# Kernel tuning notes

Hardware: AMD Instinct MI355X
Metric: run time of the kernel (lower is better)

## Reference

```python
import jax, jax.numpy as jnp
import numpy as np

IMG = 1024.0
POOL = 7
STRIDES = (4, 8, 16, 32)  # levels P2..P5
STDS = jnp.array([0.1, 0.1, 0.2, 0.2], dtype=jnp.float32)  # RCNN_TARGET_STDS


def delta2bbox(rois, deltas):
    # rois: [N,4] (y1,x1,y2,x2) pixels; deltas: [N,4]
    d = deltas * STDS  # means are zero
    y1, x1, y2, x2 = rois[:, 0], rois[:, 1], rois[:, 2], rois[:, 3]
    h = y2 - y1
    w = x2 - x1
    cy = y1 + 0.5 * h + d[:, 0] * h
    cx = x1 + 0.5 * w + d[:, 1] * w
    h = h * jnp.exp(d[:, 2])
    w = w * jnp.exp(d[:, 3])
    b = jnp.stack([cy - 0.5 * h, cx - 0.5 * w, cy + 0.5 * h, cx + 0.5 * w], axis=1)
    return jnp.clip(b, 0.0, IMG)


def crop_level(feat, rois, stride):
    # feat: [H,W,C]; bilinear 7x7 crop (crop_and_resize style)
    H, W, _ = feat.shape
    s = rois / stride
    grid = (jnp.arange(POOL, dtype=jnp.float32) + 0.5) / POOL
    ys = s[:, 0:1] + grid[None, :] * (s[:, 2:3] - s[:, 0:1])  # [N,7]
    xs = s[:, 1:2] + grid[None, :] * (s[:, 3:4] - s[:, 1:2])  # [N,7]
    y0f = jnp.clip(jnp.floor(ys), 0.0, H - 1)
    x0f = jnp.clip(jnp.floor(xs), 0.0, W - 1)
    y0 = y0f.astype(jnp.int32)
    x0 = x0f.astype(jnp.int32)
    y1 = jnp.minimum(y0 + 1, H - 1)
    x1 = jnp.minimum(x0 + 1, W - 1)
    wy = jnp.clip(ys - y0f, 0.0, 1.0)[:, :, None, None]  # [N,7,1,1]
    wx = jnp.clip(xs - x0f, 0.0, 1.0)[:, None, :, None]  # [N,1,7,1]
    g = lambda yi, xi: feat[yi[:, :, None], xi[:, None, :]]  # [N,7,7,C]
    return (g(y0, x0) * (1 - wy) * (1 - wx) + g(y0, x1) * (1 - wy) * wx
            + g(y1, x0) * wy * (1 - wx) + g(y1, x1) * wy * wx)


def pyramid_roi_align(feats, rois):
    h = rois[:, 2] - rois[:, 0]
    w = rois[:, 3] - rois[:, 1]
    lvl = jnp.floor(4.0 + jnp.log2(jnp.sqrt(jnp.maximum(h * w, 1e-6)) / 224.0))
    lvl = jnp.clip(lvl, 2.0, 5.0).astype(jnp.int32)
    pooled = 0.0
    for i, (feat, stride) in enumerate(zip(feats, STRIDES)):
        mask = (lvl == i + 2).astype(feat.dtype)[:, None, None, None]
        pooled = pooled + crop_level(feat, rois, stride) * mask
    return pooled  # [N,7,7,C]


def bbox_head(pooled, i, fc1_w, fc1_b, fc2_w, fc2_b, cls_w, cls_b, reg_w, reg_b):
    n = pooled.shape[0]
    x = pooled.reshape(n, -1)
    h1 = jax.nn.relu(x @ fc1_w[i] + fc1_b[i])
    h2 = jax.nn.relu(h1 @ fc2_w[i] + fc2_b[i])
    logits = h2 @ cls_w[i] + cls_b[i]
    probs = jax.nn.softmax(logits, axis=-1)
    deltas = h2 @ reg_w[i] + reg_b[i]
    return logits, probs, deltas


def setup_inputs() -> dict:
    key = jax.random.key(0)
    ks = jax.random.split(key, 16)
    d = {}
    for j, (name, shp) in enumerate([("P2", (1, 256, 256, 256)), ("P3", (1, 128, 128, 256)),
                                     ("P4", (1, 64, 64, 256)), ("P5", (1, 32, 32, 256))]):
        d[name] = jax.random.normal(ks[j], shp, dtype=jnp.float32)
    N = 1000
    u = jax.random.uniform(ks[4], (N, 4))
    hh = 16.0 * 2.0 ** (u[:, 0] * 5.0)  # box sizes 16..512 px, spans all pyramid levels
    ww = 16.0 * 2.0 ** (u[:, 1] * 5.0)
    y1 = u[:, 2] * (IMG - hh)
    x1 = u[:, 3] * (IMG - ww)
    d["rois"] = jnp.stack([y1, x1, y1 + hh, x1 + ww], axis=1)
    d["fc1_w"] = jax.random.normal(ks[5], (3, 12544, 1024), dtype=jnp.float32) * 0.01
    d["fc1_b"] = jnp.zeros((3, 1024), jnp.float32)
    d["fc2_w"] = jax.random.normal(ks[6], (3, 1024, 1024), dtype=jnp.float32) * 0.02
    d["fc2_b"] = jnp.zeros((3, 1024), jnp.float32)
    d["cls_w"] = jax.random.normal(ks[7], (3, 1024, 81), dtype=jnp.float32) * 0.02
    d["cls_b"] = jnp.zeros((3, 81), jnp.float32)
    d["reg_w"] = jax.random.normal(ks[8], (3, 1024, 4), dtype=jnp.float32) * 0.01
    d["reg_b"] = jnp.zeros((3, 4), jnp.float32)
    return d


def reference(P2, P3, P4, P5, rois, fc1_w, fc1_b, fc2_w, fc2_b, cls_w, cls_b, reg_w, reg_b):
    feats = [P2[0], P3[0], P4[0], P5[0]]
    params = (fc1_w, fc1_b, fc2_w, fc2_b, cls_w, cls_b, reg_w, reg_b)
    r = rois
    probs3 = None
    pooled = None
    for i in range(3):
        pooled = pyramid_roi_align(feats, r)
        _, probs3, deltas = bbox_head(pooled, i, *params)
        if i < 2:
            r = delta2bbox(r, deltas)
    # test-time ensemble: heads 1 and 2 re-applied to final pooled regions
    _, probs1, _ = bbox_head(pooled, 0, *params)
    _, probs2, _ = bbox_head(pooled, 1, *params)
    return (probs3 + probs1 + probs2) / 3.0
```

## Files before the change

kernel.cpp:

```cpp
#include <hip/hip_runtime.h>


#define BM 128
#define BN 128
#define BK 32
#define K1 12544
#define MPAD 1024
#define NROI 1000

typedef __bf16 bf16_t;
typedef bf16_t bf16x8 __attribute__((ext_vector_type(8)));
typedef float f32x4 __attribute__((ext_vector_type(4)));
typedef float f32x2 __attribute__((ext_vector_type(2)));
typedef unsigned short u16x4 __attribute__((ext_vector_type(4)));
typedef unsigned short u16x2 __attribute__((ext_vector_type(2)));

__device__ __forceinline__ unsigned short f2bf(float x) {
  unsigned u = __float_as_uint(x);
  return (unsigned short)((u + 0x7fffu + ((u >> 16) & 1u)) >> 16);
}
__device__ __forceinline__ float bf2f(unsigned short h) {
  return __uint_as_float(((unsigned)h) << 16);
}

__device__ __forceinline__ void gld_lds16(const void* g, void* l) {
  __builtin_amdgcn_global_load_lds(
      (__attribute__((address_space(1))) void*)g,
      (__attribute__((address_space(3))) void*)l, 16, 0, 0);
}

#define PHASE_SYNC() do { \
  __builtin_amdgcn_s_barrier(); \
  asm volatile("s_waitcnt lgkmcnt(0)" ::: "memory"); \
  __builtin_amdgcn_sched_barrier(0); } while(0)

#define PHASE_END() do { \
  __builtin_amdgcn_s_setprio(0); \
  __builtin_amdgcn_s_barrier(); } while(0)

template <bool SPLIT>
__global__ __launch_bounds__(256, 4)
void gemm_bf16(const unsigned short* __restrict__ Ah,
               const unsigned short* __restrict__ Al,
               long long strideA_head,
               const unsigned short* __restrict__ Bh,
               const unsigned short* __restrict__ Bl,
               long long strideB_head,
               float* __restrict__ Cpart,
               int Nh, int K, int kcSteps)
{
  __shared__ __align__(16) unsigned short sAh[BM * BK];
  __shared__ __align__(16) unsigned short sBh[BN * BK];
  __shared__ __align__(16) unsigned short sAl[SPLIT ? BM * BK : 8];
  __shared__ __align__(16) unsigned short sBl[SPLIT ? BN * BK : 8];

  const int t = threadIdx.x;
  const int ntile = Nh / BN;
  const int bm = blockIdx.x / ntile;
  const int bn = blockIdx.x % ntile;
  const int s = blockIdx.y;
  const int h = blockIdx.z;
  const int H = gridDim.z;

  const unsigned short* Ab = Ah + (size_t)h * strideA_head + (size_t)bm * BM * K;
  const unsigned short* Bb = Bh + (size_t)h * strideB_head + (size_t)bn * BN * K;
  const unsigned short* Alb = SPLIT ? (Al + (size_t)h * strideA_head + (size_t)bm * BM * K) : (const unsigned short*)0;
  const unsigned short* Blb = SPLIT ? (Bl + (size_t)h * strideB_head + (size_t)bn * BN * K) : (const unsigned short*)0;

  int k0 = s * kcSteps * BK;
  int k1 = min(K, k0 + kcSteps * BK);

  const int srow = t >> 2;
  const int gsw = ((t & 3) ^ ((srow >> 1) & 3)) * 8;
  const int lane = t & 63;
  const int wv = t >> 6;
  const int wm = (wv >> 1) * 64;
  const int wn = (wv & 1) * 64;
  const int lr = lane & 15;
  const int q = lane >> 4;
  const int sw = (lr >> 1) & 3;
  const int cA = (q ^ sw) * 8;

  f32x4 acc[4][4];
  const f32x4 z = {0.f, 0.f, 0.f, 0.f};
#pragma unroll
  for (int i = 0; i < 4; ++i)
#pragma unroll
    for (int j = 0; j < 4; ++j) acc[i][j] = z;

  for (int kk = k0; kk < k1; kk += BK) {
#pragma unroll
    for (int j = 0; j < 2; ++j) {
      int row = j * 64 + srow;
      gld_lds16(Ab + (size_t)row * K + kk + gsw, (char*)sAh + j * 4096 + t * 16);
      gld_lds16(Bb + (size_t)row * K + kk + gsw, (char*)sBh + j * 4096 + t * 16);
      if constexpr (SPLIT) {
        gld_lds16(Alb + (size_t)row * K + kk + gsw, (char*)sAl + j * 4096 + t * 16);
        gld_lds16(Blb + (size_t)row * K + kk + gsw, (char*)sBl + j * 4096 + t * 16);
      }
    }
    __syncthreads();

    bf16x8 af[4], bfr[4];
#pragma unroll
    for (int i = 0; i < 4; ++i) af[i] = *(const bf16x8*)&sAh[(wm + i * 16 + lr) * BK + cA];
#pragma unroll
    for (int j = 0; j < 4; ++j) bfr[j] = *(const bf16x8*)&sBh[(wn + j * 16 + lr) * BK + cA];
#pragma unroll
    for (int i = 0; i < 4; ++i)
#pragma unroll
      for (int j = 0; j < 4; ++j)
        acc[i][j] = __builtin_amdgcn_mfma_f32_16x16x32_bf16(af[i], bfr[j], acc[i][j], 0, 0, 0);

    if constexpr (SPLIT) {
      bf16x8 al[4], bl[4];
#pragma unroll
      for (int i = 0; i < 4; ++i) al[i] = *(const bf16x8*)&sAl[(wm + i * 16 + lr) * BK + cA];
#pragma unroll
      for (int j = 0; j < 4; ++j) bl[j] = *(const bf16x8*)&sBl[(wn + j * 16 + lr) * BK + cA];
#pragma unroll
      for (int i = 0; i < 4; ++i)
#pragma unroll
        for (int j = 0; j < 4; ++j) {
          acc[i][j] = __builtin_amdgcn_mfma_f32_16x16x32_bf16(af[i], bl[j], acc[i][j], 0, 0, 0);
          acc[i][j] = __builtin_amdgcn_mfma_f32_16x16x32_bf16(al[i], bfr[j], acc[i][j], 0, 0, 0);
        }
    }
    __syncthreads();
  }

  float* Cb = Cpart + ((size_t)(s * H + h) * MPAD + (size_t)bm * BM) * Nh + (size_t)bn * BN;
#pragma unroll
  for (int i = 0; i < 4; ++i)
#pragma unroll
    for (int j = 0; j < 4; ++j)
#pragma unroll
      for (int r = 0; r < 4; ++r) {
        int m = wm + i * 16 + q * 4 + r;
        int n = wn + j * 16 + lr;
        Cb[(size_t)m * Nh + n] = acc[i][j][r];
      }
}

#define DS_A(XB, MH) do { \
    rA[0][0]=lda_f(XB,(MH)*4+0,0); rA[0][1]=lda_f(XB,(MH)*4+0,1); \
    rA[1][0]=lda_f(XB,(MH)*4+1,0); rA[1][1]=lda_f(XB,(MH)*4+1,1); \
    rA[2][0]=lda_f(XB,(MH)*4+2,0); rA[2][1]=lda_f(XB,(MH)*4+2,1); \
    rA[3][0]=lda_f(XB,(MH)*4+3,0); rA[3][1]=lda_f(XB,(MH)*4+3,1); } while(0)

#define DS_B(XB, NH) do { \
    rB[(NH)*2+0][0]=ldb_f(XB,(NH)*2+0,0); rB[(NH)*2+0][1]=ldb_f(XB,(NH)*2+0,1); \
    rB[(NH)*2+1][0]=ldb_f(XB,(NH)*2+1,0); rB[(NH)*2+1][1]=ldb_f(XB,(NH)*2+1,1); } while(0)

#define MFMA_Q(MH, NH) do { \
  _Pragma("unroll") \
  for (int ii = 0; ii < 4; ++ii) { \
    _Pragma("unroll") \
    for (int jj = 0; jj < 2; ++jj) { \
      acc[(MH)*4+ii][(NH)*2+jj] = __builtin_amdgcn_mfma_f32_16x16x32_bf16(rA[ii][0], rB[(NH)*2+jj][0], acc[(MH)*4+ii][(NH)*2+jj], 0, 0, 0); \
      acc[(MH)*4+ii][(NH)*2+jj] = __builtin_amdgcn_mfma_f32_16x16x32_bf16(rA[ii][1], rB[(NH)*2+jj][1], acc[(MH)*4+ii][(NH)*2+jj], 0, 0, 0); \
    } } } while(0)

__global__ __launch_bounds__(512, 2)
void gemm256_bf16(const unsigned short* __restrict__ A,
                  const unsigned short* __restrict__ B,
                  float* __restrict__ Cpart,
                  int Ntot, int K, int tilesTotal)
{
  extern __shared__ char lds[];
  const int t = threadIdx.x;
  const int ntile = Ntot >> 8;
  const int bm = blockIdx.x / ntile;
  const int bn = blockIdx.x % ntile;
  const int s = blockIdx.y;
  const int S = gridDim.y;
  const int qp = tilesTotal / S, rp = tilesTotal % S;
  const int t0 = s * qp + (s < rp ? s : rp);
  const int np = qp + (s < rp ? 1 : 0);

  const unsigned short* Ab = A + (size_t)bm * 256 * K;
  const unsigned short* Bb = B + (size_t)bn * 256 * K;

  const int srow = t >> 3;
  const int sgrp = ((t & 7) ^ (srow & 7)) << 3;

  const int lane = t & 63;
  const int wv = t >> 6;
  const int wm = (wv >> 2) << 7;
  const int wn = (wv & 3) << 6;
  const int lr = lane & 15;
  const int q = lane >> 4;

  f32x4 acc[8][4];
  const f32x4 z = {0.f, 0.f, 0.f, 0.f};
#pragma unroll
  for (int i = 0; i < 8; ++i)
#pragma unroll
    for (int j = 0; j < 4; ++j) acc[i][j] = z;

  bf16x8 rA[4][2], rB[4][2];

  auto stage_tile = [&](int xbuf, int kt) {
    const size_t col = ((size_t)(t0 + kt) << 6) + sgrp;
#pragma unroll
    for (int u = 0; u < 4; ++u) {
      const unsigned short* src = (u < 2) ? Ab : Bb;
      const int rbase = ((u & 1) << 7) + srow;
      char* dst = lds + xbuf * 65536 + ((u & 2) << 14) + ((u & 1) << 14) + t * 16;
      gld_lds16(src + (size_t)rbase * K + col, dst);
      gld_lds16(src + (size_t)(rbase + 64) * K + col, dst + 8192);
    }
  };

  auto lda_f = [&](int xbuf, int i, int ks) -> bf16x8 {
    const int row = wm + (i << 4) + lr;
    const int pg = (ks * 4 + q) ^ (row & 7);
    return *(const bf16x8*)(lds + xbuf * 65536 + row * 128 + pg * 16);
  };
  auto ldb_f = [&](int xbuf, int j, int ks) -> bf16x8 {
    const int row = wn + (j << 4) + lr;
    const int pg = (ks * 4 + q) ^ (row & 7);
    return *(const bf16x8*)(lds + xbuf * 65536 + 32768 + row * 128 + pg * 16);
  };

  stage_tile(0, 0);
  if (np > 1) {
    stage_tile(1, 1);
    asm volatile("s_waitcnt vmcnt(8)" ::: "memory");
  } else {
    asm volatile("s_waitcnt vmcnt(0)" ::: "memory");
  }
  __builtin_amdgcn_s_barrier();

  for (int i = 0; i < np; ++i) {
    const int buf = i & 1;
    const bool st = (i + 2 < np);
    DS_A(buf, 0);
    DS_B(buf, 0);
    PHASE_SYNC();
    __builtin_amdgcn_s_setprio(1);
    MFMA_Q(0, 0);
    PHASE_END();
    DS_B(buf, 1);
    PHASE_SYNC();
    __builtin_amdgcn_s_setprio(1);
    MFMA_Q(0, 1);
    PHASE_END();
    DS_A(buf, 1);
    PHASE_SYNC();
    __builtin_amdgcn_s_setprio(1);
    MFMA_Q(1, 0);
    PHASE_END();
    if (st) {
      stage_tile(buf, i + 2);
      asm volatile("s_waitcnt vmcnt(8)" ::: "memory");
    } else {
      asm volatile("s_waitcnt vmcnt(0)" ::: "memory");
    }
    __builtin_amdgcn_s_barrier();
    __builtin_amdgcn_sched_barrier(0);
    __builtin_amdgcn_s_setprio(1);
    MFMA_Q(1, 1);
    __builtin_amdgcn_s_setprio(0);
  }

  float* Cb = Cpart + (size_t)s * MPAD * Ntot +
              (size_t)(bm * 256 + wm) * Ntot + bn * 256 + wn;
#pragma unroll
  for (int i = 0; i < 8; ++i)
#pragma unroll
    for (int j = 0; j < 4; ++j)
#pragma unroll
      for (int r = 0; r < 4; ++r)
        Cb[(size_t)(i * 16 + q * 4 + r) * Ntot + j * 16 + lr] = acc[i][j][r];
}

#define S_DS_A(XB, MH) do { \
    rAh[0]=s_lda(XB,0,(MH)*2+0); rAh[1]=s_lda(XB,0,(MH)*2+1); \
    rAl[0]=s_lda(XB,1,(MH)*2+0); rAl[1]=s_lda(XB,1,(MH)*2+1); } while(0)

#define S_DS_B(XB, NH) do { \
    rBh[(NH)*2+0]=s_ldb(XB,0,(NH)*2+0); rBh[(NH)*2+1]=s_ldb(XB,0,(NH)*2+1); \
    rBl[(NH)*2+0]=s_ldb(XB,1,(NH)*2+0); rBl[(NH)*2+1]=s_ldb(XB,1,(NH)*2+1); } while(0)

#define S_MFMA_Q(MH, NH) do { \
  _Pragma("unroll") \
  for (int ii = 0; ii < 2; ++ii) { \
    _Pragma("unroll") \
    for (int jj = 0; jj < 2; ++jj) { \
      f32x4* a = &acc[(MH)*2+ii][(NH)*2+jj]; \
      *a = __builtin_amdgcn_mfma_f32_16x16x32_bf16(rAh[ii], rBh[(NH)*2+jj], *a, 0, 0, 0); \
      *a = __builtin_amdgcn_mfma_f32_16x16x32_bf16(rAh[ii], rBl[(NH)*2+jj], *a, 0, 0, 0); \
      *a = __builtin_amdgcn_mfma_f32_16x16x32_bf16(rAl[ii], rBh[(NH)*2+jj], *a, 0, 0, 0); \
    } } } while(0)

__global__ __launch_bounds__(512, 2)
void gemm256s_bf16(const unsigned short* __restrict__ Ah,
                   const unsigned short* __restrict__ Al,
                   const unsigned short* __restrict__ Bh,
                   const unsigned short* __restrict__ Bl,
                   float* __restrict__ Cpart,
                   int Ntot, int K, int tilesTotal)
{
  extern __shared__ char lds[];
  const int t = threadIdx.x;
  const int ntile = Ntot >> 8;
  const int bm = blockIdx.x / ntile;
  const int bn = blockIdx.x % ntile;
  const int s = blockIdx.y;
  const int S = gridDim.y;
  const int qp = tilesTotal / S, rp = tilesTotal % S;
  const int t0 = s * qp + (s < rp ? s : rp);
  const int np = qp + (s < rp ? 1 : 0);

  const unsigned short* Ahb = Ah + (size_t)bm * 128 * K;
  const unsigned short* Alb = Al + (size_t)bm * 128 * K;
  const unsigned short* Bhb = Bh + (size_t)bn * 256 * K;
  const unsigned short* Blb = Bl + (size_t)bn * 256 * K;

  const int srow = t >> 2;
  const int sgrp = ((t & 3) ^ ((srow >> 1) & 3)) << 3;

  const int lane = t & 63;
  const int wv = t >> 6;
  const int wm = (wv >> 2) << 6;
  const int wn = (wv & 3) << 6;
  const int lr = lane & 15;
  const int q = lane >> 4;

  f32x4 acc[4][4];
  const f32x4 z = {0.f, 0.f, 0.f, 0.f};
#pragma unroll
  for (int i = 0; i < 4; ++i)
#pragma unroll
    for (int j = 0; j < 4; ++j) acc[i][j] = z;

  bf16x8 rAh[2], rAl[2], rBh[4], rBl[4];

  auto stage_tile = [&](int xbuf, int kt) {
    const size_t col = ((size_t)(t0 + kt) << 5) + sgrp;
    char* base = lds + xbuf * 49152;
    gld_lds16(Ahb + (size_t)srow * K + col, base + t * 16);
    gld_lds16(Alb + (size_t)srow * K + col, base + 8192 + t * 16);
    gld_lds16(Bhb + (size_t)srow * K + col, base + 16384 + t * 16);
    gld_lds16(Bhb + (size_t)(srow + 128) * K + col, base + 16384 + 8192 + t * 16);
    gld_lds16(Blb + (size_t)srow * K + col, base + 32768 + t * 16);
    gld_lds16(Blb + (size_t)(srow + 128) * K + col, base + 32768 + 8192 + t * 16);
  };

  auto s_lda = [&](int xbuf, int pl, int i) -> bf16x8 {
    const int row = wm + (i << 4) + lr;
    const int pg = q ^ ((row >> 1) & 3);
    return *(const bf16x8*)(lds + xbuf * 49152 + pl * 8192 + row * 64 + pg * 16);
  };
  auto s_ldb = [&](int xbuf, int pl, int j) -> bf16x8 {
    const int row = wn + (j << 4) + lr;
    const int pg = q ^ ((row >> 1) & 3);
    return *(const bf16x8*)(lds + xbuf * 49152 + 16384 + pl * 16384 + row * 64 + pg * 16);
  };

  stage_tile(0, 0);
  if (np > 1) {
    stage_tile(1, 1);
    asm volatile("s_waitcnt vmcnt(6)" ::: "memory");
  } else {
    asm volatile("s_waitcnt vmcnt(0)" ::: "memory");
  }
  __builtin_amdgcn_s_barrier();

  for (int i = 0; i < np; ++i) {
    const int buf = i & 1;
    const bool st = (i + 2 < np);
    S_DS_A(buf, 0);
    S_DS_B(buf, 0);
    PHASE_SYNC();
    __builtin_amdgcn_s_setprio(1);
    S_MFMA_Q(0, 0);
    PHASE_END();
    S_DS_B(buf, 1);
    PHASE_SYNC();
    __builtin_amdgcn_s_setprio(1);
    S_MFMA_Q(0, 1);
    PHASE_END();
    S_DS_A(buf, 1);
    PHASE_SYNC();
    __builtin_amdgcn_s_setprio(1);
    S_MFMA_Q(1, 0);
    PHASE_END();
    if (st) {
      stage_tile(buf, i + 2);
      asm volatile("s_waitcnt vmcnt(6)" ::: "memory");
    } else {
      asm volatile("s_waitcnt vmcnt(0)" ::: "memory");
    }
    __builtin_amdgcn_s_barrier();
    __builtin_amdgcn_sched_barrier(0);
    __builtin_amdgcn_s_setprio(1);
    S_MFMA_Q(1, 1);
    __builtin_amdgcn_s_setprio(0);
  }

  float* Cb = Cpart + (size_t)s * MPAD * Ntot +
              (size_t)(bm * 128 + wm) * Ntot + bn * 256 + wn;
#pragma unroll
  for (int i = 0; i < 4; ++i)
#pragma unroll
    for (int j = 0; j < 4; ++j)
#pragma unroll
      for (int r = 0; r < 4; ++r)
        Cb[(size_t)(i * 16 + q * 4 + r) * Ntot + j * 16 + lr] = acc[i][j][r];
}

__global__ __launch_bounds__(256)
void epilogue_kernel(const float* __restrict__ Cpart, int S, int H, int Nh,
                     const float* __restrict__ bias,
                     unsigned short* __restrict__ ohi,
                     unsigned short* __restrict__ olo, int flags)
{
  size_t total = (size_t)H * MPAD * Nh;
  size_t idx = ((size_t)blockIdx.x * 256 + threadIdx.x) * 4;
  if (idx >= total) return;
  int n = (int)(idx % Nh);
  int h = (int)(idx / ((size_t)MPAD * Nh));
  f32x4 v = *(const f32x4*)&bias[(size_t)h * Nh + n];
  for (int s = 0; s < S; ++s) v += *(const f32x4*)&Cpart[(size_t)s * total + idx];
  u16x4 hi, lo;
#pragma unroll
  for (int j = 0; j < 4; ++j) {
    float x = fmaxf(v[j], 0.f);
    hi[j] = f2bf(x);
    lo[j] = f2bf(x - bf2f(hi[j]));
  }
  *(u16x4*)&ohi[idx] = hi;
  if (flags & 4) *(u16x4*)&olo[idx] = lo;
}

__global__ __launch_bounds__(256)
void epilogue_fc1_s2(const float* __restrict__ Cpart, int S,
                     const float* __restrict__ bias,
                     unsigned short* __restrict__ ohi)
{
  const size_t total = (size_t)MPAD * 3072;
  size_t idx = ((size_t)blockIdx.x * 256 + threadIdx.x) * 4;
  if (idx >= total) return;
  int n = (int)(idx % 3072);
  int m = (int)(idx / 3072);
  f32x4 v = *(const f32x4*)&bias[n];
  for (int s = 0; s < S; ++s) v += *(const f32x4*)&Cpart[(size_t)s * total + idx];
  u16x4 hi;
#pragma unroll
  for (int j = 0; j < 4; ++j) hi[j] = f2bf(fmaxf(v[j], 0.f));
  int h = n >> 10;
  *(u16x4*)&ohi[((size_t)h * MPAD + m) * 1024 + (n & 1023)] = hi;
}

__global__ __launch_bounds__(256)
void transpose_convert(const float* __restrict__ W,
                       unsigned short* __restrict__ Thi,
                       unsigned short* __restrict__ Tlo,
                       int K, int N, int loHeads)
{
  __shared__ float tile[32][260];
  int kb = blockIdx.x * 256;
  int nb = blockIdx.y * 32;
  int h = blockIdx.z;
  const float* Wb = W + (size_t)h * K * N + (size_t)kb * N + nb;
  int tn = threadIdx.x & 31;
  int tk = threadIdx.x >> 5;
#pragma unroll
  for (int i = 0; i < 32; ++i) {
    int k = tk + i * 8;
    tile[tn][k] = Wb[(size_t)k * N + tn];
  }
  __syncthreads();
  bool wlo = h < loHeads;
  int l = threadIdx.x & 63;
  int ng = threadIdx.x >> 6;
  size_t ob = (size_t)h * N * K + (size_t)nb * K + kb;
#pragma unroll
  for (int i = 0; i < 8; ++i) {
    int n = ng + i * 4;
    f32x4 v = *(const f32x4*)&tile[n][4 * l];
    u16x4 hi;
#pragma unroll
    for (int j = 0; j < 4; ++j) hi[j] = f2bf(v[j]);
    *(u16x4*)&Thi[ob + (size_t)n * K + 4 * l] = hi;
    if (wlo) {
      u16x4 lo;
#pragma unroll
      for (int j = 0; j < 4; ++j) lo[j] = f2bf(v[j] - bf2f(hi[j]));
      *(u16x4*)&Tlo[ob + (size_t)n * K + 4 * l] = lo;
    }
  }
}

__global__ void transpose_cls(const float* __restrict__ W, unsigned short* __restrict__ T)
{
  int n = blockIdx.x, h = blockIdx.y, t = threadIdx.x;
  size_t ob = ((size_t)h * 128 + n) * 1024;
  if (n < 81) {
    for (int k = t; k < 1024; k += 256)
      T[ob + k] = f2bf(W[((size_t)h * 1024 + k) * 81 + n]);
  } else {
    for (int k = t; k < 1024; k += 256) T[ob + k] = 0;
  }
}

__global__ void roi_align_kernel(const float* __restrict__ rois,
                                 const float* __restrict__ P2, const float* __restrict__ P3,
                                 const float* __restrict__ P4, const float* __restrict__ P5,
                                 unsigned short* __restrict__ phi,
                                 unsigned short* __restrict__ plo, int writeLo)
{
  int m = blockIdx.x;
  int t = threadIdx.x;
  int c = (t & 63) * 4;
  int pg = t >> 6;
  const float* rp = rois + m * 4;
  float y1 = rp[0], x1 = rp[1], y2 = rp[2], x2 = rp[3];
  float hh = y2 - y1, ww = x2 - x1;
  float a = sqrtf(fmaxf(hh * ww, 1e-6f)) / 224.0f;
  float lvl = floorf(4.0f + log2f(a));
  lvl = fminf(fmaxf(lvl, 2.0f), 5.0f);
  int i = (int)lvl - 2;
  const float* f = (i == 0) ? P2 : (i == 1) ? P3 : (i == 2) ? P4 : P5;
  int H = 256 >> i;
  float stride = (float)(4 << i);
  float sy1 = y1 / stride, sx1 = x1 / stride;
  float dy = y2 / stride - sy1, dx = x2 / stride - sx1;
  size_t base = (size_t)m * K1 + c;
  for (int p = pg; p < 49; p += 4) {
    int py = p / 7, px = p % 7;
    float ys = sy1 + ((py + 0.5f) / 7.0f) * dy;
    float xs = sx1 + ((px + 0.5f) / 7.0f) * dx;
    float y0f = fminf(fmaxf(floorf(ys), 0.0f), (float)(H - 1));
    float x0f = fminf(fmaxf(floorf(xs), 0.0f), (float)(H - 1));
    int y0 = (int)y0f, x0 = (int)x0f;
    int y1i = min(y0 + 1, H - 1), x1i = min(x0 + 1, H - 1);
    float wy = fminf(fmaxf(ys - y0f, 0.0f), 1.0f);
    float wx = fminf(fmaxf(xs - x0f, 0.0f), 1.0f);
    f32x4 v00 = *(const f32x4*)(f + ((size_t)y0 * H + x0) * 256 + c);
    f32x4 v01 = *(const f32x4*)(f + ((size_t)y0 * H + x1i) * 256 + c);
    f32x4 v10 = *(const f32x4*)(f + ((size_t)y1i * H + x0) * 256 + c);
    f32x4 v11 = *(const f32x4*)(f + ((size_t)y1i * H + x1i) * 256 + c);
    float w00 = (1.f - wy) * (1.f - wx), w01 = (1.f - wy) * wx;
    float w10 = wy * (1.f - wx), w11 = wy * wx;
    f32x4 v = v00 * w00 + v01 * w01 + v10 * w10 + v11 * w11;
    u16x4 hi;
#pragma unroll
    for (int j = 0; j < 4; ++j) hi[j] = f2bf(v[j]);
    *(u16x4*)&phi[base + p * 256] = hi;
    if (writeLo) {
      u16x4 lo;
#pragma unroll
      for (int j = 0; j < 4; ++j) lo[j] = f2bf(v[j] - bf2f(hi[j]));
      *(u16x2*)&plo[base + p * 256] = *(u16x2*)&lo;
      *(u16x2*)&plo[base + p * 256 + 2] = *((u16x2*)&lo + 1);
    }
  }
}

__global__ void reg_delta_kernel(const float* __restrict__ Cpart, int S,
                                 const float* __restrict__ fb,
                                 const float* __restrict__ rw, const float* __restrict__ rb,
                                 const float* __restrict__ rin, float* __restrict__ rout)
{
  int m = blockIdx.x, t = threadIdx.x;
  float s0 = 0, s1 = 0, s2 = 0, s3 = 0;
  for (int n = t; n < 1024; n += 256) {
    float v = fb[n];
    for (int s = 0; s < S; ++s) v += Cpart[((size_t)s * 1024 + m) * 1024 + n];
    v = fmaxf(v, 0.f);
    const float* w = rw + (size_t)n * 4;
    s0 += v * w[0]; s1 += v * w[1]; s2 += v * w[2]; s3 += v * w[3];
  }
#pragma unroll
  for (int o = 32; o > 0; o >>= 1) {
    s0 += __shfl_xor(s0, o, 64);
    s1 += __shfl_xor(s1, o, 64);
    s2 += __shfl_xor(s2, o, 64);
    s3 += __shfl_xor(s3, o, 64);
  }
  __shared__ float part[4][4];
  int w = t >> 6;
  if ((t & 63) == 0) { part[w][0] = s0; part[w][1] = s1; part[w][2] = s2; part[w][3] = s3; }
  __syncthreads();
  if (t == 0) {
    float d0 = (part[0][0] + part[1][0] + part[2][0] + part[3][0] + rb[0]) * 0.1f;
    float d1 = (part[0][1] + part[1][1] + part[2][1] + part[3][1] + rb[1]) * 0.1f;
    float d2 = (part[0][2] + part[1][2] + part[2][2] + part[3][2] + rb[2]) * 0.2f;
    float d3 = (part[0][3] + part[1][3] + part[2][3] + part[3][3] + rb[3]) * 0.2f;
    const float* r = rin + m * 4;
    float y1 = r[0], x1 = r[1], y2 = r[2], x2 = r[3];
    float h = y2 - y1, wd = x2 - x1;
    float cy = y1 + 0.5f * h + d0 * h;
    float cx = x1 + 0.5f * wd + d1 * wd;
    float nh = h * expf(d2);
    float nw = wd * expf(d3);
    float* ro = rout + m * 4;
    ro[0] = fminf(fmaxf(cy - 0.5f * nh, 0.f), 1024.f);
    ro[1] = fminf(fmaxf(cx - 0.5f * nw, 0.f), 1024.f);
    ro[2] = fminf(fmaxf(cy + 0.5f * nh, 0.f), 1024.f);
    ro[3] = fminf(fmaxf(cx + 0.5f * nw, 0.f), 1024.f);
  }
}

__global__ void softmax_avg_kernel(const float* __restrict__ Cpart, int S,
                                   const float* __restrict__ cls_b,
                                   float* __restrict__ out)
{
  int m = blockIdx.x, t = threadIdx.x;
  __shared__ float sh[128];
  float pacc = 0.0f;
  for (int h = 0; h < 3; ++h) {
    float x = -3.0e38f;
    if (t < 81) {
      x = cls_b[h * 81 + t];
      for (int s = 0; s < S; ++s)
        x += Cpart[((size_t)(s * 3 + h) * 1024 + m) * 128 + t];
    }
    sh[t] = x; __syncthreads();
    for (int o = 64; o > 0; o >>= 1) { if (t < o) sh[t] = fmaxf(sh[t], sh[t + o]); __syncthreads(); }
    float mx = sh[0]; __syncthreads();
    float e = (t < 81) ? expf(x - mx) : 0.0f;
    sh[t] = e; __syncthreads();
    for (int o = 64; o > 0; o >>= 1) { if (t < o) sh[t] += sh[t + o]; __syncthreads(); }
    float sum = sh[0]; __syncthreads();
    pacc += e / sum;
  }
  if (t < 81) out[(size_t)m * 81 + t] = pacc / 3.0f;
}

extern "C" void kernel_launch(void* const* d_in, const int* in_sizes, int n_in,
                              void* d_out, int out_size, void* d_ws, size_t ws_size,
                              hipStream_t stream)
{
  const float* P2 = (const float*)d_in[0];
  const float* P3 = (const float*)d_in[1];
  const float* P4 = (const float*)d_in[2];
  const float* P5 = (const float*)d_in[3];
  const float* rois = (const float*)d_in[4];
  const float* fc1_w = (const float*)d_in[5];
  const float* fc1_b = (const float*)d_in[6];
  const float* fc2_w = (const float*)d_in[7];
  const float* fc2_b = (const float*)d_in[8];
  const float* cls_w = (const float*)d_in[9];
  const float* cls_b = (const float*)d_in[10];
  const float* reg_w = (const float*)d_in[11];
  const float* reg_b = (const float*)d_in[12];
  float* out = (float*)d_out;

  char* ws = (char*)d_ws;
  size_t off = 0;
  auto alloc = [&](size_t b) -> char* {
    char* p = ws + off;
    off = (off + b + 255) & ~(size_t)255;
    return p;
  };
  unsigned short* w1t_hi = (unsigned short*)alloc(3ull * 1024 * K1 * 2);
  unsigned short* w2t_hi = (unsigned short*)alloc(3ull * 1024 * 1024 * 2);
  unsigned short* w2t_lo = (unsigned short*)alloc(2ull * 1024 * 1024 * 2);
  unsigned short* w3t    = (unsigned short*)alloc(3ull * 128 * 1024 * 2);
  unsigned short* phi    = (unsigned short*)alloc((size_t)MPAD * K1 * 2);
  unsigned short* plo    = (unsigned short*)alloc((size_t)MPAD * K1 * 2);
  unsigned short* h1_hi  = (unsigned short*)alloc(3ull * MPAD * 1024 * 2);
  unsigned short* h1_lo  = (unsigned short*)alloc((size_t)MPAD * 1024 * 2);
  unsigned short* h2_hi  = (unsigned short*)alloc(3ull * MPAD * 1024 * 2);
  float* r1              = (float*)alloc(16384);
  float* r2              = (float*)alloc(16384);
  const size_t w1lo_bytes = 2ull * 1024 * K1 * 2;
  unsigned short* w1t_lo = (unsigned short*)alloc(w1lo_bytes);

  const size_t SLAB = (size_t)MPAD * 1024 * 4;
  size_t tail = (ws_size > off) ? (ws_size - off) : 0;

  int S01 = (int)(tail / SLAB);
  if (S01 > 8) S01 = 8;
  if (S01 < 1) S01 = 1;
  float* cpart01 = (float*)(ws + off);
  const int S2 = 4;
  float* cpart2 = (float*)w1t_lo;

  const int fc2Steps01 = (32 + S01 - 1) / S01;

  const long long hs1 = (long long)1024 * K1;
  const long long hs2 = (long long)1024 * 1024;

  dim3 b256(256);

  hipLaunchKernelGGL(transpose_convert, dim3(K1 / 256, 32, 3), b256, 0, stream,
                     fc1_w, w1t_hi, w1t_lo, K1, 1024, 2);
  hipLaunchKernelGGL(transpose_convert, dim3(4, 32, 3), b256, 0, stream,
                     fc2_w, w2t_hi, w2t_lo, 1024, 1024, 2);
  hipLaunchKernelGGL(transpose_cls, dim3(128, 3), b256, 0, stream, cls_w, w3t);
  hipMemsetAsync(phi + (size_t)NROI * K1, 0, (size_t)(MPAD - NROI) * K1 * 2, stream);
  hipMemsetAsync(plo + (size_t)NROI * K1, 0, (size_t)(MPAD - NROI) * K1 * 2, stream);

  for (int st = 0; st < 2; ++st) {
    const float* rin = (st == 0) ? rois : r1;
    float* rout = (st == 0) ? r1 : r2;
    hipLaunchKernelGGL(roi_align_kernel, dim3(NROI), b256, 0, stream,
                       rin, P2, P3, P4, P5, phi, plo, 1);
    hipLaunchKernelGGL(gemm256s_bf16, dim3(32, S01), dim3(512), 98304, stream,
                       phi, plo,
                       w1t_hi + (size_t)st * hs1, w1t_lo + (size_t)st * hs1,
                       cpart01, 1024, K1, 392);
    hipLaunchKernelGGL(epilogue_kernel, dim3(1024), b256, 0, stream,
                       cpart01, S01, 1, 1024, fc1_b + st * 1024,
                       h1_hi, h1_lo, 4);
    hipLaunchKernelGGL((gemm_bf16<true>), dim3(64, S01, 1), b256, 0, stream,
                       h1_hi, h1_lo, 0LL,
                       w2t_hi + (size_t)st * hs2, w2t_lo + (size_t)st * hs2, 0LL,
                       cpart01, 1024, 1024, fc2Steps01);
    hipLaunchKernelGGL(reg_delta_kernel, dim3(NROI), b256, 0, stream,
                       cpart01, S01, fc2_b + st * 1024,
                       reg_w + (size_t)st * 1024 * 4, reg_b + st * 4,
                       rin, rout);
  }

  hipLaunchKernelGGL(roi_align_kernel, dim3(NROI), b256, 0, stream,
                     r2, P2, P3, P4, P5, phi, plo, 0);
  {
    const size_t SLAB3 = (size_t)MPAD * 3072 * 4;
    size_t availC2 = ws_size - (size_t)((char*)w1t_lo - ws);
    int S2f = 5;
    while (S2f > 1 && (size_t)S2f * SLAB3 > availC2) --S2f;
    hipLaunchKernelGGL(gemm256_bf16, dim3(48, S2f), dim3(512), 131072, stream,
                       phi, w1t_hi, cpart2, 3072, K1, 196);
    hipLaunchKernelGGL(epilogue_fc1_s2, dim3(3072), b256, 0, stream,
                       cpart2, S2f, fc1_b, h1_hi);
  }
  hipLaunchKernelGGL((gemm_bf16<false>), dim3(64, S2, 3), b256, 0, stream,
                     h1_hi, (const unsigned short*)0, hs2,
                     w2t_hi, (const unsigned short*)0, hs2,
                     cpart2, 1024, 1024, (32 + S2 - 1) / S2);
  hipLaunchKernelGGL(epilogue_kernel, dim3(3072), b256, 0, stream,
                     cpart2, S2, 3, 1024, fc2_b,
                     h2_hi, (unsigned short*)0, 0);
  hipLaunchKernelGGL((gemm_bf16<false>), dim3(8, 8, 3), b256, 0, stream,
                     h2_hi, (const unsigned short*)0, hs2,
                     w3t, (const unsigned short*)0, (long long)128 * 1024,
                     cpart2, 128, 1024, 4);
  hipLaunchKernelGGL(softmax_avg_kernel, dim3(NROI), dim3(128), 0, stream,
                     cpart2, 8, cls_b, out);
}
```

Measured before the change: 786.7 us.

## Double-buffer LDS fragments in registers across k-tiles in split-K GEMM

Rewrites the main loop of gemm256s_bf16 so each k-tile's A/B hi/lo fragments are read from LDS into one register set while MFMAs run on the other. The loop is unrolled by two so the sets alternate. This drops the four intra-tile phase syncs in favour of one LDS wait and barrier per tile, aiming to overlap LDS reads with MFMA work. It doubles the fragment registers held live, which under the 512-thread, 2-blocks-per-CU launch bound risks spills or lower occupancy.

```diff
diff --git a/kernel.cpp b/kernel.cpp
--- a/kernel.cpp
+++ b/kernel.cpp
@@ -275,24 +275,43 @@
         Cb[(size_t)(i * 16 + q * 4 + r) * Ntot + j * 16 + lr] = acc[i][j][r];
 }
 
-#define S_DS_A(XB, MH) do { \
-    rAh[0]=s_lda(XB,0,(MH)*2+0); rAh[1]=s_lda(XB,0,(MH)*2+1); \
-    rAl[0]=s_lda(XB,1,(MH)*2+0); rAl[1]=s_lda(XB,1,(MH)*2+1); } while(0)
-
-#define S_DS_B(XB, NH) do { \
-    rBh[(NH)*2+0]=s_ldb(XB,0,(NH)*2+0); rBh[(NH)*2+1]=s_ldb(XB,0,(NH)*2+1); \
-    rBl[(NH)*2+0]=s_ldb(XB,1,(NH)*2+0); rBl[(NH)*2+1]=s_ldb(XB,1,(NH)*2+1); } while(0)
-
-#define S_MFMA_Q(MH, NH) do { \
+#define S_LOADSET(XB, SUF) do { \
   _Pragma("unroll") \
-  for (int ii = 0; ii < 2; ++ii) { \
+  for (int k_ = 0; k_ < 4; ++k_) { \
+    aH##SUF[k_] = s_lda((XB), 0, k_); \
+    aL##SUF[k_] = s_lda((XB), 1, k_); \
+    bH##SUF[k_] = s_ldb((XB), 0, k_); \
+    bL##SUF[k_] = s_ldb((XB), 1, k_); \
+  } } while (0)
+
+#define S_MFMASET(SUF) do { \
+  _Pragma("unroll") \
+  for (int i_ = 0; i_ < 4; ++i_) { \
     _Pragma("unroll") \
-    for (int jj = 0; jj < 2; ++jj) { \
-      f32x4* a = &acc[(MH)*2+ii][(NH)*2+jj]; \
-      *a = __builtin_amdgcn_mfma_f32_16x16x32_bf16(rAh[ii], rBh[(NH)*2+jj], *a, 0, 0, 0); \
-      *a = __builtin_amdgcn_mfma_f32_16x16x32_bf16(rAh[ii], rBl[(NH)*2+jj], *a, 0, 0, 0); \
-      *a = __builtin_amdgcn_mfma_f32_16x16x32_bf16(rAl[ii], rBh[(NH)*2+jj], *a, 0, 0, 0); \
-    } } } while(0)
+    for (int j_ = 0; j_ < 4; ++j_) { \
+      f32x4* a_ = &acc[i_][j_]; \
+      *a_ = __builtin_amdgcn_mfma_f32_16x16x32_bf16(aH##SUF[i_], bH##SUF[j_], *a_, 0, 0, 0); \
+      *a_ = __builtin_amdgcn_mfma_f32_16x16x32_bf16(aH##SUF[i_], bL##SUF[j_], *a_, 0, 0, 0); \
+      *a_ = __builtin_amdgcn_mfma_f32_16x16x32_bf16(aL##SUF[i_], bH##SUF[j_], *a_, 0, 0, 0); \
+    } } } while (0)
+
+#define S_TILE(I, CUR, OTH) do { \
+  const bool st_ = ((I) + 2 < np); \
+  if (st_) { \
+    stage_tile((CUR), (I) + 2); \
+    asm volatile("s_waitcnt vmcnt(6)" ::: "memory"); \
+  } else { \
+    asm volatile("s_waitcnt vmcnt(0)" ::: "memory"); \
+  } \
+  __builtin_amdgcn_s_barrier(); \
+  if ((I) + 1 < np) { S_LOADSET((CUR) ^ 1, OTH); } \
+  __builtin_amdgcn_s_setprio(1); \
+  S_MFMASET(CUR); \
+  __builtin_amdgcn_s_setprio(0); \
+  asm volatile("s_waitcnt lgkmcnt(0)" ::: "memory"); \
+  __builtin_amdgcn_sched_barrier(0); \
+  __builtin_amdgcn_s_barrier(); \
+} while (0)
 
 __global__ __launch_bounds__(512, 2)
 void gemm256s_bf16(const unsigned short* __restrict__ Ah,
@@ -335,7 +354,8 @@
 #pragma unroll
     for (int j = 0; j < 4; ++j) acc[i][j] = z;
 
-  bf16x8 rAh[2], rAl[2], rBh[4], rBl[4];
+  bf16x8 aH0[4], aL0[4], bH0[4], bL0[4];
+  bf16x8 aH1[4], aL1[4], bH1[4], bL1[4];
 
   auto stage_tile = [&](int xbuf, int kt) {
     const size_t col = ((size_t)(t0 + kt) << 5) + sgrp;
@@ -367,48 +387,27 @@
     asm volatile("s_waitcnt vmcnt(0)" ::: "memory");
   }
   __builtin_amdgcn_s_barrier();
-
-  for (int i = 0; i < np; ++i) {
-    const int buf = i & 1;
-    const bool st = (i + 2 < np);
-    S_DS_A(buf, 0);
-    S_DS_B(buf, 0);
-    PHASE_SYNC();
-    __builtin_amdgcn_s_setprio(1);
-    S_MFMA_Q(0, 0);
-    PHASE_END();
-    S_DS_B(buf, 1);
-    PHASE_SYNC();
-    __builtin_amdgcn_s_setprio(1);
-    S_MFMA_Q(0, 1);
-    PHASE_END();
-    S_DS_A(buf, 1);
-    PHASE_SYNC();
-    __builtin_amdgcn_s_setprio(1);
-    S_MFMA_Q(1, 0);
-    PHASE_END();
-    if (st) {
-      stage_tile(buf, i + 2);
-      asm volatile("s_waitcnt vmcnt(6)" ::: "memory");
-    } else {
-      asm volatile("s_waitcnt vmcnt(0)" ::: "memory");
-    }
-    __builtin_amdgcn_s_barrier();
-    __builtin_amdgcn_sched_barrier(0);
-    __builtin_amdgcn_s_setprio(1);
-    S_MFMA_Q(1, 1);
-    __builtin_amdgcn_s_setprio(0);
-  }
+  S_LOADSET(0, 0);
+  asm volatile("s_waitcnt lgkmcnt(0)" ::: "memory");
+  __builtin_amdgcn_sched_barrier(0);
+  __builtin_amdgcn_s_barrier();
+
+  int i = 0;
+  for (; i + 2 <= np; i += 2) {
+    S_TILE(i, 0, 1);
+    S_TILE(i + 1, 1, 0);
+  }
+  if (i < np) S_TILE(i, 0, 1);
 
   float* Cb = Cpart + (size_t)s * MPAD * Ntot +
               (size_t)(bm * 128 + wm) * Ntot + bn * 256 + wn;
 #pragma unroll
-  for (int i = 0; i < 4; ++i)
-#pragma unroll
-    for (int j = 0; j < 4; ++j)
+  for (int ii = 0; ii < 4; ++ii)
+#pragma unroll
+    for (int jj = 0; jj < 4; ++jj)
 #pragma unroll
       for (int r = 0; r < 4; ++r)
-        Cb[(size_t)(i * 16 + q * 4 + r) * Ntot + j * 16 + lr] = acc[i][j][r];
+        Cb[(size_t)(ii * 16 + q * 4 + r) * Ntot + jj * 16 + lr] = acc[ii][jj][r];
 }
 
 __global__ __launch_bounds__(256)
```

New measurement: 783.7 us. No clear change (-0.4%).
